# Kernel tuning notes

Measured on AMD Instinct MI355X. Metric: run time of the kernel, lower is better.

Reference implementation:

```python
import jax, jax.numpy as jnp
import numpy as np

D_H, HEAD, LAYER_IDX = 1024, 16, 11
D_ATTN = D_H // HEAD
BZ, LEN = 2, 2048


def setup_inputs() -> dict:
    key = jax.random.key(0)
    ks = jax.random.split(key, 8)
    s = 1.0 / np.sqrt(D_H)
    v = jax.random.normal(ks[0], (BZ, LEN, D_H), jnp.float32)
    k = jax.random.normal(ks[1], (BZ, LEN, D_H), jnp.float32)
    q = jax.random.normal(ks[2], (BZ, LEN, D_H), jnp.float32)
    # causal mask: 1.0 where attention is blocked (j > i)
    causal = jnp.triu(jnp.ones((LEN, LEN), jnp.float32), k=1)
    mask = jnp.broadcast_to(causal[None, None], (BZ, 1, LEN, LEN))
    Wv = jax.random.normal(ks[3], (D_H, D_H), jnp.float32) * s
    Wk = jax.random.normal(ks[4], (D_H, D_H), jnp.float32) * s
    Wq = jax.random.normal(ks[5], (D_H, D_H), jnp.float32) * s
    Wo = jax.random.normal(ks[6], (D_H, D_H), jnp.float32) * s
    bo = jnp.zeros((D_H,), jnp.float32)
    return {"v": v, "k": k, "q": q, "mask": mask,
            "Wv": Wv, "Wk": Wk, "Wq": Wq, "Wo": Wo, "bo": bo}


def _split_head(x):
    # (bz, len, d_h) -> (bz, head, len, d_attn)
    bz, L, _ = x.shape
    return x.reshape(bz, L, HEAD, D_ATTN).transpose(0, 2, 1, 3)


def reference(v, k, q, mask, Wv, Wk, Wq, Wo, bo):
    bz, len_q, _ = q.shape
    vh = _split_head(v @ Wv)  # (bz, head, len_k, d_attn)
    kh = _split_head(k @ Wk)
    qh = _split_head(q @ Wq)
    scale = 1.0 / jnp.sqrt(jnp.asarray(D_ATTN, jnp.float32))
    weight = jnp.einsum("bhqd,bhkd->bhqk", qh, kh) * scale
    weight = weight + mask * (-1e9)
    weight = weight / jnp.asarray(LAYER_IDX + 1, jnp.float32)
    attn = jax.nn.softmax(weight, axis=-1)  # dropout omitted (inference)
    out = jnp.einsum("bhqk,bhkd->bhqd", attn, vh)
    out = out.transpose(0, 2, 1, 3).reshape(bz, len_q, D_H)
    return out @ Wo + bo
```

## Files before the change

### kernel.cpp

```cpp
#include <hip/hip_runtime.h>
#include <hip/hip_fp16.h>

typedef _Float16 f16;
typedef _Float16 f16x4 __attribute__((ext_vector_type(4)));
typedef _Float16 f16x8 __attribute__((ext_vector_type(8)));
typedef float f32x4 __attribute__((ext_vector_type(4)));

#define D_H   1024
#define LEN   2048
#define BZ    2
#define NHEAD 16
#define DA    64
#define MTOK  (BZ * LEN)
#define KDIM  1024
#define ATT_SCALE (0.125f / 12.0f)

__device__ __forceinline__ void load_lds16(const f16* g, f16* l) {
  __builtin_amdgcn_global_load_lds((const __attribute__((address_space(1))) void*)g,
                                   (__attribute__((address_space(3))) void*)l,
                                   16, 0, 0);
}

__global__ __launch_bounds__(256)
void k_transpose4(const float* __restrict__ W0, const float* __restrict__ W1,
                  const float* __restrict__ W2, const float* __restrict__ W3,
                  f16* __restrict__ T0, f16* __restrict__ T1,
                  f16* __restrict__ T2, f16* __restrict__ T3) {
  int z = blockIdx.z;
  const float* W = (z == 0) ? W0 : (z == 1) ? W1 : (z == 2) ? W2 : W3;
  f16* Wt = (z == 0) ? T0 : (z == 1) ? T1 : (z == 2) ? T2 : T3;
  __shared__ float tile[32][33];
  int bx = blockIdx.x, by = blockIdx.y;
  int tx = threadIdx.x, ty = threadIdx.y;
#pragma unroll
  for (int s = 0; s < 4; ++s)
    tile[ty + 8 * s][tx] = W[(size_t)(by * 32 + ty + 8 * s) * D_H + bx * 32 + tx];
  __syncthreads();
#pragma unroll
  for (int s = 0; s < 4; ++s)
    Wt[(size_t)(bx * 32 + ty + 8 * s) * D_H + by * 32 + tx] =
        (f16)tile[tx][ty + 8 * s];
}

#define BM 128
#define BN 128
#define BK 64
__global__ __launch_bounds__(256)
void k_gemm3(const float* __restrict__ A0, const float* __restrict__ A1,
             const float* __restrict__ A2, const f16* __restrict__ W0,
             const f16* __restrict__ W1, const f16* __restrict__ W2,
             f16* __restrict__ O0, f16* __restrict__ O1, f16* __restrict__ O2) {
  __shared__ __align__(16) char smem[(BM + BN) * BK * 2];
  f16* As = (f16*)smem;
  f16* Bs = As + BM * BK;
  const int z = blockIdx.z;
  const float* A = (z == 0) ? A0 : (z == 1) ? A1 : A2;
  const f16* Bt = (z == 0) ? W0 : (z == 1) ? W1 : W2;
  f16* Out = (z == 0) ? O0 : (z == 1) ? O1 : O2;
  const int m0 = blockIdx.x * BM, n0 = blockIdx.y * BN;
  const int tid = threadIdx.x;
  const int wave = tid >> 6, lane = tid & 63;
  const int lc = lane & 15, quad = lane >> 4;
  const int wm = (wave >> 1) * 64, wn = (wave & 1) * 64;
  const int swz = lc & 7;
  const float* Ab = A + (size_t)m0 * KDIM;
  const f16* Bb = Bt + (size_t)n0 * KDIM;

  f32x4 acc[4][4] = {};

  for (int k0 = 0; k0 < KDIM; k0 += BK) {
#pragma unroll
    for (int r = 0; r < 4; ++r) {
      int idx = tid + r * 256;
      int row = idx >> 3, ch = idx & 7;
      int gch = ch ^ (row & 7);
      const float* src = Ab + (size_t)row * KDIM + k0 + gch * 8;
      float4 x0 = *(const float4*)src;
      float4 x1 = *(const float4*)(src + 4);
      f16x8 hh;
      hh[0] = (f16)x0.x; hh[1] = (f16)x0.y; hh[2] = (f16)x0.z; hh[3] = (f16)x0.w;
      hh[4] = (f16)x1.x; hh[5] = (f16)x1.y; hh[6] = (f16)x1.z; hh[7] = (f16)x1.w;
      *(f16x8*)&As[idx * 8] = hh;
    }
#pragma unroll
    for (int r = 0; r < 4; ++r) {
      int idx = tid + r * 256;
      int row = idx >> 3, ch = idx & 7;
      int gch = ch ^ (row & 7);
      load_lds16(Bb + (size_t)row * KDIM + k0 + gch * 8, &Bs[idx * 8]);
    }
    __syncthreads();
#pragma unroll
    for (int kc = 0; kc < 2; ++kc) {
      f16x8 af[4], bf[4];
#pragma unroll
      for (int mi = 0; mi < 4; ++mi)
        af[mi] = *(const f16x8*)&As[(wm + mi * 16 + lc) * 64 +
                                    (((kc * 4 + quad) ^ swz) * 8)];
#pragma unroll
      for (int ni = 0; ni < 4; ++ni)
        bf[ni] = *(const f16x8*)&Bs[(wn + ni * 16 + lc) * 64 +
                                    (((kc * 4 + quad) ^ swz) * 8)];
#pragma unroll
      for (int mi = 0; mi < 4; ++mi)
#pragma unroll
        for (int ni = 0; ni < 4; ++ni)
          acc[mi][ni] = __builtin_amdgcn_mfma_f32_16x16x32_f16(
              af[mi], bf[ni], acc[mi][ni], 0, 0, 0);
    }
    __syncthreads();
  }

  if (z <= 1) {
    f16* Ct = (f16*)smem;
#pragma unroll
    for (int hf = 0; hf < 2; ++hf) {
      __syncthreads();
      if ((wave & 1) == hf) {
#pragma unroll
        for (int mi = 0; mi < 4; ++mi)
#pragma unroll
          for (int ni = 0; ni < 4; ++ni)
#pragma unroll
            for (int r = 0; r < 4; ++r) {
              int tok = wm + mi * 16 + quad * 4 + r;
              int d = ni * 16 + lc;
              Ct[tok * 72 + d] = (f16)acc[mi][ni][r];
            }
      }
      __syncthreads();
      int hA = (n0 >> 6) + hf;
#pragma unroll
      for (int it = 0; it < 4; ++it) {
        int u = tid + it * 256;
        int tok = u >> 3, ch = u & 7;
        int gm = m0 + tok;
        int b = gm >> 11, i = gm & 2047;
        f16x8 vv = *(const f16x8*)&Ct[tok * 72 + ch * 8];
        *(f16x8*)(Out + ((size_t)((b << 4) + hA) * LEN + i) * DA + ch * 8) = vv;
      }
    }
  } else {
    f16* Ct = (f16*)smem;
    const int b = m0 >> 11, j0m = m0 & 2047;
#pragma unroll
    for (int hf = 0; hf < 2; ++hf) {
      __syncthreads();
      if ((wave & 1) == hf) {
#pragma unroll
        for (int mi = 0; mi < 4; ++mi)
#pragma unroll
          for (int ni = 0; ni < 4; ++ni)
#pragma unroll
            for (int r = 0; r < 4; ++r) {
              int tok = wm + mi * 16 + quad * 4 + r;
              int d = ni * 16 + lc;
              Ct[d * 136 + tok] = (f16)acc[mi][ni][r];
            }
      }
      __syncthreads();
      int hA = (n0 >> 6) + hf;
#pragma unroll
      for (int it = 0; it < 4; ++it) {
        int u = tid + it * 256;
        int d = u >> 4, ch = u & 15;
        f16x8 vv = *(const f16x8*)&Ct[d * 136 + ch * 8];
        *(f16x8*)(Out + ((size_t)((b << 4) + hA) * DA + d) * LEN + j0m + ch * 8) = vv;
      }
    }
  }
}

#define OM 64
#define ON 128
#define ONIT (KDIM / BK)
__global__ __launch_bounds__(256)
void k_gemm_out(const f16* __restrict__ A, const f16* __restrict__ Bt,
                float* __restrict__ Out, const float* __restrict__ bias) {
  __shared__ __align__(16) char smem[2 * (OM + ON) * BK * 2];
  f16* As = (f16*)smem;
  f16* Bs = As + 2 * OM * BK;
  const int m0 = blockIdx.x * OM, n0 = blockIdx.y * ON;
  const int tid = threadIdx.x;
  const int wave = tid >> 6, lane = tid & 63;
  const int lc = lane & 15, quad = lane >> 4;
  const int wm = (wave >> 1) * 32, wn = (wave & 1) * 64;
  const int swz = lc & 7;
  const f16* Abase = A + (size_t)m0 * KDIM;
  const f16* Bbase = Bt + (size_t)n0 * KDIM;

  f32x4 acc[2][4] = {};

#define STAGE_OUT(t)                                                          \
  {                                                                           \
    int k0s = (t) * BK;                                                       \
    f16* Ad = As + ((t) & 1) * (OM * BK);                                     \
    f16* Bd = Bs + ((t) & 1) * (ON * BK);                                     \
    _Pragma("unroll")                                                         \
    for (int r = 0; r < 2; ++r) {                                             \
      int idx = tid + r * 256;                                                \
      int row = idx >> 3, ch = idx & 7;                                       \
      int gch = ch ^ (row & 7);                                               \
      load_lds16(Abase + (size_t)row * KDIM + k0s + gch * 8, &Ad[idx * 8]);   \
    }                                                                         \
    _Pragma("unroll")                                                         \
    for (int r = 0; r < 4; ++r) {                                             \
      int idx = tid + r * 256;                                                \
      int row = idx >> 3, ch = idx & 7;                                       \
      int gch = ch ^ (row & 7);                                               \
      load_lds16(Bbase + (size_t)row * KDIM + k0s + gch * 8, &Bd[idx * 8]);   \
    }                                                                         \
  }

  STAGE_OUT(0);
  for (int t = 0; t < ONIT; ++t) {
    __syncthreads();
    if (t + 1 < ONIT) STAGE_OUT(t + 1);
    const f16* Ad = As + (t & 1) * (OM * BK);
    const f16* Bd = Bs + (t & 1) * (ON * BK);
#pragma unroll
    for (int kc = 0; kc < 2; ++kc) {
      f16x8 af[2], bf[4];
#pragma unroll
      for (int mi = 0; mi < 2; ++mi)
        af[mi] = *(const f16x8*)&Ad[(wm + mi * 16 + lc) * 64 +
                                    (((kc * 4 + quad) ^ swz) * 8)];
#pragma unroll
      for (int ni = 0; ni < 4; ++ni)
        bf[ni] = *(const f16x8*)&Bd[(wn + ni * 16 + lc) * 64 +
                                    (((kc * 4 + quad) ^ swz) * 8)];
#pragma unroll
      for (int mi = 0; mi < 2; ++mi)
#pragma unroll
        for (int ni = 0; ni < 4; ++ni)
          acc[mi][ni] = __builtin_amdgcn_mfma_f32_16x16x32_f16(
              af[mi], bf[ni], acc[mi][ni], 0, 0, 0);
    }
  }

  float* Ct = (float*)smem;
#pragma unroll
  for (int hf = 0; hf < 2; ++hf) {
    __syncthreads();
    if ((wave & 1) == hf) {
#pragma unroll
      for (int mi = 0; mi < 2; ++mi)
#pragma unroll
        for (int ni = 0; ni < 4; ++ni)
#pragma unroll
          for (int r = 0; r < 4; ++r) {
            int tok = wm + mi * 16 + quad * 4 + r;
            int d = ni * 16 + lc;
            Ct[tok * 68 + d] = acc[mi][ni][r];
          }
    }
    __syncthreads();
#pragma unroll
    for (int it = 0; it < 4; ++it) {
      int u = tid + it * 256;
      int tok = u >> 4, ch = u & 15;
      int gm = m0 + tok;
      int gc = n0 + hf * 64 + ch * 4;
      float4 bv = *(const float4*)(bias + gc);
      float4 cv = *(const float4*)&Ct[tok * 68 + ch * 4];
      float4 ov;
      ov.x = cv.x + bv.x; ov.y = cv.y + bv.y;
      ov.z = cv.z + bv.z; ov.w = cv.w + bv.w;
      *(float4*)(Out + (size_t)gm * D_H + gc) = ov;
    }
  }
}

__global__ __launch_bounds__(256, 4)
void k_attn(const f16* __restrict__ Qh, const f16* __restrict__ Kh,
            const f16* __restrict__ Vt, f16* __restrict__ O16) {
  __shared__ f16 Ks[2][64 * 64];
  __shared__ f16 Vs[2][64 * 64];
  __shared__ f16 Pw[4][16 * 64];
  const int tid = threadIdx.x;
  const int wave = tid >> 6, lane = tid & 63;
  const int lc = lane & 15, quad = lane >> 4;
  const int swz = lc & 7;
  const int bh = blockIdx.x & 31;
  const int qb = 31 - (blockIdx.x >> 5);
  const int i0 = qb * 64 + wave * 16;
  const int b = bh >> 4, h = bh & 15;
  const f16* Qb = Qh + (size_t)bh * LEN * DA;
  const f16* Kb = Kh + (size_t)bh * LEN * DA;
  const f16* Vb = Vt + (size_t)bh * DA * LEN;

  f16x8 aQ[2];
  const f16 qs = (f16)ATT_SCALE;
#pragma unroll
  for (int c = 0; c < 2; ++c) {
    aQ[c] = *(const f16x8*)(Qb + (size_t)(i0 + lc) * DA + c * 32 + quad * 8);
#pragma unroll
    for (int j = 0; j < 8; ++j) aQ[c][j] = aQ[c][j] * qs;
  }

  float lsum = 0.f;
  f32x4 accO[4] = {};
  f16* P = &Pw[wave][0];

  const int niter = qb + 1;

#pragma unroll
  for (int r = 0; r < 2; ++r) {
    int idx = tid + r * 256;
    int row = idx >> 3, ch = idx & 7;
    int gch = ch ^ (row & 7);
    load_lds16(Kb + (size_t)row * DA + gch * 8, &Ks[0][idx * 8]);
  }
#pragma unroll
  for (int r = 0; r < 2; ++r) {
    int idx = tid + r * 256;
    int row = idx >> 3, ch = idx & 7;
    int gch = ch ^ (row & 7);
    load_lds16(Vb + (size_t)row * LEN + gch * 8, &Vs[0][idx * 8]);
  }

  for (int t = 0; t < niter; ++t) {
    __syncthreads();
    if (t + 1 < niter) {
      int j0n = (t + 1) * 64, nb = (t + 1) & 1;
#pragma unroll
      for (int r = 0; r < 2; ++r) {
        int idx = tid + r * 256;
        int row = idx >> 3, ch = idx & 7;
        int gch = ch ^ (row & 7);
        load_lds16(Kb + (size_t)(j0n + row) * DA + gch * 8, &Ks[nb][idx * 8]);
      }
#pragma unroll
      for (int r = 0; r < 2; ++r) {
        int idx = tid + r * 256;
        int row = idx >> 3, ch = idx & 7;
        int gch = ch ^ (row & 7);
        load_lds16(Vb + (size_t)row * LEN + j0n + gch * 8, &Vs[nb][idx * 8]);
      }
    }
    const f16* ks = Ks[t & 1];
    const f16* vs = Vs[t & 1];

    f32x4 st[4] = {};
#pragma unroll
    for (int g = 0; g < 4; ++g)
#pragma unroll
      for (int c = 0; c < 2; ++c) {
        f16x8 aK = *(const f16x8*)&ks[(g * 16 + lc) * 64 +
                                      (((c * 4 + quad) ^ swz) * 8)];
        st[g] = __builtin_amdgcn_mfma_f32_16x16x32_f16(aK, aQ[c], st[g], 0, 0, 0);
      }
    float ev[4][4];
    if (t == niter - 1) {
      const int j0 = t * 64, q = i0 + lc;
#pragma unroll
      for (int g = 0; g < 4; ++g)
#pragma unroll
        for (int r = 0; r < 4; ++r) {
          int key = j0 + g * 16 + quad * 4 + r;
          float e = __expf(st[g][r]);
          e = (key > q) ? 0.f : e;
          lsum += e;
          ev[g][r] = e;
        }
    } else {
#pragma unroll
      for (int g = 0; g < 4; ++g)
#pragma unroll
        for (int r = 0; r < 4; ++r) {
          float e = __expf(st[g][r]);
          lsum += e;
          ev[g][r] = e;
        }
    }
#pragma unroll
    for (int g = 0; g < 4; ++g) {
      int c8 = ((g << 1) + (quad >> 1)) ^ swz;
      f16x4 pk;
      pk[0] = (f16)ev[g][0]; pk[1] = (f16)ev[g][1];
      pk[2] = (f16)ev[g][2]; pk[3] = (f16)ev[g][3];
      *(f16x4*)&P[lc * 64 + c8 * 8 + (quad & 1) * 4] = pk;
    }
    __asm__ volatile("s_waitcnt lgkmcnt(0)" ::: "memory");
    f16x8 aP[2];
#pragma unroll
    for (int c = 0; c < 2; ++c) {
      int c8 = (quad + 4 * c) ^ swz;
      aP[c] = *(const f16x8*)&P[lc * 64 + c8 * 8];
    }
#pragma unroll
    for (int dc = 0; dc < 4; ++dc) {
      f16x8 bV0 = *(const f16x8*)&vs[(dc * 16 + lc) * 64 + ((quad ^ swz) * 8)];
      f16x8 bV1 = *(const f16x8*)&vs[(dc * 16 + lc) * 64 + (((4 + quad) ^ swz) * 8)];
      accO[dc] = __builtin_amdgcn_mfma_f32_16x16x32_f16(aP[0], bV0, accO[dc], 0, 0, 0);
      accO[dc] = __builtin_amdgcn_mfma_f32_16x16x32_f16(aP[1], bV1, accO[dc], 0, 0, 0);
    }
  }

  lsum += __shfl_xor(lsum, 16, 64);
  lsum += __shfl_xor(lsum, 32, 64);
  float ls[4];
#pragma unroll
  for (int r = 0; r < 4; ++r) ls[r] = __shfl(lsum, quad * 4 + r, 64);

#pragma unroll
  for (int dc = 0; dc < 4; ++dc)
#pragma unroll
    for (int r = 0; r < 4; ++r) {
      int i = i0 + quad * 4 + r;
      int d = dc * 16 + lc;
      float v = accO[dc][r] / ls[r];
      O16[((size_t)(b * LEN + i)) * D_H + h * DA + d] = (f16)v;
    }
}

extern "C" void kernel_launch(void* const* d_in, const int* in_sizes, int n_in,
                              void* d_out, int out_size, void* d_ws, size_t ws_size,
                              hipStream_t stream) {
  const float* v_f = (const float*)d_in[0];
  const float* k_f = (const float*)d_in[1];
  const float* q_f = (const float*)d_in[2];
  const float* Wv = (const float*)d_in[4];
  const float* Wk = (const float*)d_in[5];
  const float* Wq = (const float*)d_in[6];
  const float* Wo = (const float*)d_in[7];
  const float* bo = (const float*)d_in[8];
  float* out = (float*)d_out;

  const size_t SZ_X = (size_t)MTOK * D_H;
  const size_t SZ_W = (size_t)D_H * D_H;
  f16* ws = (f16*)d_ws;
  f16* Qh  = ws;
  f16* Kh  = ws + SZ_X;
  f16* Vt  = ws + 2 * SZ_X;
  f16* O16 = ws + 3 * SZ_X;
  f16* Wqt = ws + 4 * SZ_X;
  f16* Wkt = Wqt + SZ_W;
  f16* Wvt = Wqt + 2 * SZ_W;
  f16* Wot = Wqt + 3 * SZ_W;

  k_transpose4<<<dim3(32, 32, 4), dim3(32, 8), 0, stream>>>(
      Wq, Wk, Wv, Wo, Wqt, Wkt, Wvt, Wot);

  k_gemm3<<<dim3(MTOK / BM, D_H / BN, 3), 256, 0, stream>>>(
      q_f, k_f, v_f, Wqt, Wkt, Wvt, Qh, Kh, Vt);

  k_attn<<<dim3(32 * 32), 256, 0, stream>>>(Qh, Kh, Vt, O16);

  k_gemm_out<<<dim3(MTOK / OM, D_H / ON), 256, 0, stream>>>(O16, Wot, out, bo);
}
```

Measured before the change: 232.6 us.

## Pre-convert activations to fp16 and double-buffer QKV GEMM with async LDS loads

Adds a prep pass that converts the fp32 q/k/v activations to fp16 in the same launch as the weight transposes. The QKV projection GEMM can then load A via direct global-to-LDS loads and use a double-buffered BK=32 pipeline with one barrier per iteration, instead of converting fp32 to fp16 in registers every K step. This costs an extra write and read of the fp16 activations in global memory and a larger workspace, with O16 aliasing the q16 buffer.

```diff
diff --git a/kernel.cpp b/kernel.cpp
--- a/kernel.cpp
+++ b/kernel.cpp
@@ -22,39 +22,57 @@
 }
 
 __global__ __launch_bounds__(256)
-void k_transpose4(const float* __restrict__ W0, const float* __restrict__ W1,
-                  const float* __restrict__ W2, const float* __restrict__ W3,
-                  f16* __restrict__ T0, f16* __restrict__ T1,
-                  f16* __restrict__ T2, f16* __restrict__ T3) {
-  int z = blockIdx.z;
-  const float* W = (z == 0) ? W0 : (z == 1) ? W1 : (z == 2) ? W2 : W3;
-  f16* Wt = (z == 0) ? T0 : (z == 1) ? T1 : (z == 2) ? T2 : T3;
-  __shared__ float tile[32][33];
-  int bx = blockIdx.x, by = blockIdx.y;
-  int tx = threadIdx.x, ty = threadIdx.y;
-#pragma unroll
-  for (int s = 0; s < 4; ++s)
-    tile[ty + 8 * s][tx] = W[(size_t)(by * 32 + ty + 8 * s) * D_H + bx * 32 + tx];
-  __syncthreads();
-#pragma unroll
-  for (int s = 0; s < 4; ++s)
-    Wt[(size_t)(bx * 32 + ty + 8 * s) * D_H + by * 32 + tx] =
-        (f16)tile[tx][ty + 8 * s];
+void k_prep(const float* __restrict__ W0, const float* __restrict__ W1,
+            const float* __restrict__ W2, const float* __restrict__ W3,
+            const float* __restrict__ xq, const float* __restrict__ xk,
+            const float* __restrict__ xv,
+            f16* __restrict__ T0, f16* __restrict__ T1,
+            f16* __restrict__ T2, f16* __restrict__ T3,
+            f16* __restrict__ q16, f16* __restrict__ k16,
+            f16* __restrict__ v16) {
+  const int z = blockIdx.z;
+  const int tx = threadIdx.x, ty = threadIdx.y;
+  if (z < 4) {
+    const float* W = (z == 0) ? W0 : (z == 1) ? W1 : (z == 2) ? W2 : W3;
+    f16* Wt = (z == 0) ? T0 : (z == 1) ? T1 : (z == 2) ? T2 : T3;
+    __shared__ float tile[32][33];
+    int bx = blockIdx.x, by = blockIdx.y;
+#pragma unroll
+    for (int s = 0; s < 4; ++s)
+      tile[ty + 8 * s][tx] = W[(size_t)(by * 32 + ty + 8 * s) * D_H + bx * 32 + tx];
+    __syncthreads();
+#pragma unroll
+    for (int s = 0; s < 4; ++s)
+      Wt[(size_t)(bx * 32 + ty + 8 * s) * D_H + by * 32 + tx] =
+          (f16)tile[tx][ty + 8 * s];
+  } else {
+    const float* in = (z == 4) ? xq : (z == 5) ? xk : xv;
+    f16* out = (z == 4) ? q16 : (z == 5) ? k16 : v16;
+    int tid = ty * 32 + tx;
+    size_t base = ((size_t)(blockIdx.y * 32 + blockIdx.x)) * 4096 + tid * 16;
+#pragma unroll
+    for (int s = 0; s < 4; ++s) {
+      float4 x = *(const float4*)(in + base + s * 4);
+      f16x4 o; o[0] = (f16)x.x; o[1] = (f16)x.y; o[2] = (f16)x.z; o[3] = (f16)x.w;
+      *(f16x4*)(out + base + s * 4) = o;
+    }
+  }
 }
 
 #define BM 128
 #define BN 128
-#define BK 64
+#define BK3 32
+#define NIT3 (KDIM / BK3)
 __global__ __launch_bounds__(256)
-void k_gemm3(const float* __restrict__ A0, const float* __restrict__ A1,
-             const float* __restrict__ A2, const f16* __restrict__ W0,
+void k_gemm3(const f16* __restrict__ A0, const f16* __restrict__ A1,
+             const f16* __restrict__ A2, const f16* __restrict__ W0,
              const f16* __restrict__ W1, const f16* __restrict__ W2,
              f16* __restrict__ O0, f16* __restrict__ O1, f16* __restrict__ O2) {
-  __shared__ __align__(16) char smem[(BM + BN) * BK * 2];
+  __shared__ __align__(16) char smem[32768];
   f16* As = (f16*)smem;
-  f16* Bs = As + BM * BK;
+  f16* Bs = As + 2 * BM * BK3;
   const int z = blockIdx.z;
-  const float* A = (z == 0) ? A0 : (z == 1) ? A1 : A2;
+  const f16* A = (z == 0) ? A0 : (z == 1) ? A1 : A2;
   const f16* Bt = (z == 0) ? W0 : (z == 1) ? W1 : W2;
   f16* Out = (z == 0) ? O0 : (z == 1) ? O1 : O2;
   const int m0 = blockIdx.x * BM, n0 = blockIdx.y * BN;
@@ -62,53 +80,55 @@
   const int wave = tid >> 6, lane = tid & 63;
   const int lc = lane & 15, quad = lane >> 4;
   const int wm = (wave >> 1) * 64, wn = (wave & 1) * 64;
-  const int swz = lc & 7;
-  const float* Ab = A + (size_t)m0 * KDIM;
+  const f16* Ab = A + (size_t)m0 * KDIM;
   const f16* Bb = Bt + (size_t)n0 * KDIM;
 
   f32x4 acc[4][4] = {};
 
-  for (int k0 = 0; k0 < KDIM; k0 += BK) {
-#pragma unroll
-    for (int r = 0; r < 4; ++r) {
-      int idx = tid + r * 256;
-      int row = idx >> 3, ch = idx & 7;
-      int gch = ch ^ (row & 7);
-      const float* src = Ab + (size_t)row * KDIM + k0 + gch * 8;
-      float4 x0 = *(const float4*)src;
-      float4 x1 = *(const float4*)(src + 4);
-      f16x8 hh;
-      hh[0] = (f16)x0.x; hh[1] = (f16)x0.y; hh[2] = (f16)x0.z; hh[3] = (f16)x0.w;
-      hh[4] = (f16)x1.x; hh[5] = (f16)x1.y; hh[6] = (f16)x1.z; hh[7] = (f16)x1.w;
-      *(f16x8*)&As[idx * 8] = hh;
-    }
-#pragma unroll
-    for (int r = 0; r < 4; ++r) {
-      int idx = tid + r * 256;
-      int row = idx >> 3, ch = idx & 7;
-      int gch = ch ^ (row & 7);
-      load_lds16(Bb + (size_t)row * KDIM + k0 + gch * 8, &Bs[idx * 8]);
-    }
-    __syncthreads();
-#pragma unroll
-    for (int kc = 0; kc < 2; ++kc) {
-      f16x8 af[4], bf[4];
-#pragma unroll
-      for (int mi = 0; mi < 4; ++mi)
-        af[mi] = *(const f16x8*)&As[(wm + mi * 16 + lc) * 64 +
-                                    (((kc * 4 + quad) ^ swz) * 8)];
+#define STAGE3(t)                                                             \
+  {                                                                           \
+    int k0s = (t) * BK3;                                                      \
+    f16* Ad = As + ((t) & 1) * (BM * BK3);                                    \
+    f16* Bd = Bs + ((t) & 1) * (BN * BK3);                                    \
+    _Pragma("unroll")                                                         \
+    for (int r = 0; r < 2; ++r) {                                             \
+      int idx = tid + r * 256;                                                \
+      int row = idx >> 2, ch = idx & 3;                                       \
+      int gch = ch ^ ((row >> 1) & 3);                                        \
+      load_lds16(Ab + (size_t)row * KDIM + k0s + gch * 8, &Ad[idx * 8]);      \
+    }                                                                         \
+    _Pragma("unroll")                                                         \
+    for (int r = 0; r < 2; ++r) {                                             \
+      int idx = tid + r * 256;                                                \
+      int row = idx >> 2, ch = idx & 3;                                       \
+      int gch = ch ^ ((row >> 1) & 3);                                        \
+      load_lds16(Bb + (size_t)row * KDIM + k0s + gch * 8, &Bd[idx * 8]);      \
+    }                                                                         \
+  }
+
+  STAGE3(0);
+  for (int t = 0; t < NIT3; ++t) {
+    __syncthreads();
+    if (t + 1 < NIT3) STAGE3(t + 1);
+    const f16* Ad = As + (t & 1) * (BM * BK3);
+    const f16* Bd = Bs + (t & 1) * (BN * BK3);
+    f16x8 af[4], bf[4];
+#pragma unroll
+    for (int mi = 0; mi < 4; ++mi) {
+      int row = wm + mi * 16 + lc;
+      af[mi] = *(const f16x8*)&Ad[(row * 4 + (quad ^ ((row >> 1) & 3))) * 8];
+    }
+#pragma unroll
+    for (int ni = 0; ni < 4; ++ni) {
+      int row = wn + ni * 16 + lc;
+      bf[ni] = *(const f16x8*)&Bd[(row * 4 + (quad ^ ((row >> 1) & 3))) * 8];
+    }
+#pragma unroll
+    for (int mi = 0; mi < 4; ++mi)
 #pragma unroll
       for (int ni = 0; ni < 4; ++ni)
-        bf[ni] = *(const f16x8*)&Bs[(wn + ni * 16 + lc) * 64 +
-                                    (((kc * 4 + quad) ^ swz) * 8)];
-#pragma unroll
-      for (int mi = 0; mi < 4; ++mi)
-#pragma unroll
-        for (int ni = 0; ni < 4; ++ni)
-          acc[mi][ni] = __builtin_amdgcn_mfma_f32_16x16x32_f16(
-              af[mi], bf[ni], acc[mi][ni], 0, 0, 0);
-    }
-    __syncthreads();
+        acc[mi][ni] = __builtin_amdgcn_mfma_f32_16x16x32_f16(
+            af[mi], bf[ni], acc[mi][ni], 0, 0, 0);
   }
 
   if (z <= 1) {
@@ -173,6 +193,7 @@
 
 #define OM 64
 #define ON 128
+#define BK 64
 #define ONIT (KDIM / BK)
 __global__ __launch_bounds__(256)
 void k_gemm_out(const f16* __restrict__ A, const f16* __restrict__ Bt,
@@ -430,20 +451,23 @@
   const size_t SZ_X = (size_t)MTOK * D_H;
   const size_t SZ_W = (size_t)D_H * D_H;
   f16* ws = (f16*)d_ws;
-  f16* Qh  = ws;
-  f16* Kh  = ws + SZ_X;
-  f16* Vt  = ws + 2 * SZ_X;
-  f16* O16 = ws + 3 * SZ_X;
-  f16* Wqt = ws + 4 * SZ_X;
+  f16* q16 = ws;
+  f16* k16 = ws + SZ_X;
+  f16* v16 = ws + 2 * SZ_X;
+  f16* Qh  = ws + 3 * SZ_X;
+  f16* Kh  = ws + 4 * SZ_X;
+  f16* Vt  = ws + 5 * SZ_X;
+  f16* Wqt = ws + 6 * SZ_X;
   f16* Wkt = Wqt + SZ_W;
   f16* Wvt = Wqt + 2 * SZ_W;
   f16* Wot = Wqt + 3 * SZ_W;
-
-  k_transpose4<<<dim3(32, 32, 4), dim3(32, 8), 0, stream>>>(
-      Wq, Wk, Wv, Wo, Wqt, Wkt, Wvt, Wot);
+  f16* O16 = q16;
+
+  k_prep<<<dim3(32, 32, 7), dim3(32, 8), 0, stream>>>(
+      Wq, Wk, Wv, Wo, q_f, k_f, v_f, Wqt, Wkt, Wvt, Wot, q16, k16, v16);
 
   k_gemm3<<<dim3(MTOK / BM, D_H / BN, 3), 256, 0, stream>>>(
-      q_f, k_f, v_f, Wqt, Wkt, Wvt, Qh, Kh, Vt);
+      q16, k16, v16, Wqt, Wkt, Wvt, Qh, Kh, Vt);
 
   k_attn<<<dim3(32 * 32), 256, 0, stream>>>(Qh, Kh, Vt, O16);
 
```

Result: faster. 220.0 us (-5.4%).
